# Kernel tuning notes

Hardware: AMD Instinct MI355X
Metric: run time of the kernel (lower is better)

The kernel has to match this reference:

```python
import jax, jax.numpy as jnp
import numpy as np

B, C, H, Wd = 256, 2048, 14, 14
E, A = 16, 3000  # num experts (DESC_INDEX), num answers (ANSWER_INDEX)


def setup_inputs() -> dict:
    key = jax.random.key(0)
    k1, k2, k3, k4, k5 = jax.random.split(key, 5)
    return {
        "mask": jax.random.uniform(k1, (B, 1, H, Wd), dtype=jnp.float32),
        "features": jax.random.normal(k2, (B, C, H, Wd), dtype=jnp.float32),
        "W": jax.random.normal(k3, (E, A, C), dtype=jnp.float32) * 0.02,
        "b": jax.random.normal(k4, (E, A), dtype=jnp.float32) * 0.02,
        "inst": jax.random.randint(k5, (B,), 0, E, dtype=jnp.int64),
    }


def reference(mask, features, W, b, inst):
    Bn, Cn = features.shape[0], features.shape[1]
    feat = features.reshape(Bn, Cn, -1)          # [B, C, HW]
    m = mask.reshape(Bn, 1, -1) + 1e-10          # [B, 1, HW]
    # masked weighted average pool over spatial positions
    attended = (m * feat).sum(2) / m.sum(2)      # [B, C]
    # per-sample expert Linear: compute all experts via one GEMM, then gather
    logits = jnp.einsum('bc,eac->bea', attended, W) + b[None]  # [B, E, A]
    out = jnp.take_along_axis(logits, inst[:, None, None], axis=1)[:, 0, :]  # [B, A]
    return out
```

## Files before the change

kernel.cpp:

```cpp
#include <hip/hip_runtime.h>
#include <cstdint>

#define BN   256
#define CN   2048
#define HWN  196
#define EN   16
#define AN   3000

#define TS   32
#define TA   64
#define KC   32
#define LDST 36
#define KSPLIT 4
#define KPART (CN / KSPLIT)

#define RPW  8

__global__ __launch_bounds__(256) void den_kernel(const float* __restrict__ mask,
                                                  float* __restrict__ rden) {
    int wave = blockIdx.x * 4 + (threadIdx.x >> 6);
    int lane = threadIdx.x & 63;
    float den = 0.f;
    if (lane < HWN / 4) {
        float4 m = ((const float4*)(mask + (size_t)wave * HWN))[lane];
        den = (m.x + 1e-10f) + (m.y + 1e-10f) + (m.z + 1e-10f) + (m.w + 1e-10f);
    }
    #pragma unroll
    for (int off = 32; off; off >>= 1) den += __shfl_xor(den, off, 64);
    if (lane == 0) rden[wave] = 1.0f / den;
}

__global__ __launch_bounds__(256) void pool_kernel(const float* __restrict__ mask,
                                                   const float* __restrict__ feat,
                                                   const float* __restrict__ rden,
                                                   float* __restrict__ attended) {
    int wave = blockIdx.x * 4 + (threadIdx.x >> 6);
    int lane = threadIdx.x & 63;
    int b  = wave >> 8;
    int c0 = (wave & 255) * RPW;
    bool act = lane < HWN / 4;

    float4 m = make_float4(0.f, 0.f, 0.f, 0.f);
    if (act) {
        m = ((const float4*)(mask + (size_t)b * HWN))[lane];
        m.x += 1e-10f; m.y += 1e-10f; m.z += 1e-10f; m.w += 1e-10f;
    }
    const float4* fb = (const float4*)(feat + ((size_t)b * CN + c0) * HWN);
    float4 f[RPW];
    #pragma unroll
    for (int r = 0; r < RPW; r++)
        f[r] = act ? fb[r * (HWN / 4) + lane] : make_float4(0.f, 0.f, 0.f, 0.f);
    float num[RPW];
    #pragma unroll
    for (int r = 0; r < RPW; r++)
        num[r] = m.x * f[r].x + m.y * f[r].y + m.z * f[r].z + m.w * f[r].w;
    #pragma unroll
    for (int off = 32; off; off >>= 1)
        #pragma unroll
        for (int r = 0; r < RPW; r++) num[r] += __shfl_xor(num[r], off, 64);
    if (lane == 0) {
        float rd = rden[b];
        #pragma unroll
        for (int r = 0; r < RPW; r++)
            attended[(size_t)b * CN + c0 + r] = num[r] * rd;
    }
}

__global__ void group_kernel(const int* __restrict__ inst,
                             int* __restrict__ counts,
                             int* __restrict__ lists) {
    __shared__ int cnt[EN];
    int t = threadIdx.x;
    if (t < EN) cnt[t] = 0;
    __syncthreads();
    if (t < BN) {
        int e = inst[t];
        int pos = atomicAdd(&cnt[e], 1);
        lists[e * BN + pos] = t;
    }
    __syncthreads();
    if (t < EN) counts[t] = cnt[t];
}

__global__ __launch_bounds__(256) void bias_init_kernel(const float* __restrict__ bias,
                                                        const int* __restrict__ inst,
                                                        float* __restrict__ out) {
    int b = blockIdx.x;
    int e = inst[b];
    const float4* br = (const float4*)(bias + (size_t)e * AN);
    float4* orow = (float4*)(out + (size_t)b * AN);
    for (int j = threadIdx.x; j < AN / 4; j += 256) orow[j] = br[j];
}

__global__ __launch_bounds__(128, 4) void gemm_kernel(const float* __restrict__ attended,
                                                      const float* __restrict__ W,
                                                      const int* __restrict__ counts,
                                                      const int* __restrict__ lists,
                                                      float* __restrict__ out) {
    int e  = blockIdx.y;
    int kp = blockIdx.z;
    int a0 = blockIdx.x * TA;
    int n  = counts[e];
    if (n == 0) return;
    int kbeg = kp * KPART;
    int kend = kbeg + KPART;

    __shared__ float At[TS * LDST];
    __shared__ float Wt[TA * LDST];
    __shared__ int   sid[TS];

    int t    = threadIdx.x;
    int ts   = t & 7;
    int ta   = t >> 3;
    int srow = t >> 3;
    int spos = t & 7;
    const int* lst = lists + e * BN;

    for (int s0 = 0; s0 < n; s0 += TS) {
        if (t < TS) sid[t] = (s0 + t < n) ? lst[s0 + t] : -1;

        float acc[4][4];
        #pragma unroll
        for (int i = 0; i < 4; i++)
            #pragma unroll
            for (int j = 0; j < 4; j++) acc[i][j] = 0.f;

        __syncthreads();

        float4 apre[2], wpre[4];
        #pragma unroll
        for (int r = 0; r < 2; r++) {
            int s = sid[srow + 16 * r];
            apre[r] = make_float4(0.f, 0.f, 0.f, 0.f);
            if (s >= 0)
                apre[r] = *(const float4*)(attended + (size_t)s * CN + kbeg + spos * 4);
        }
        #pragma unroll
        for (int r = 0; r < 4; r++) {
            int a = a0 + srow + 16 * r; if (a > AN - 1) a = AN - 1;
            wpre[r] = *(const float4*)(W + ((size_t)e * AN + a) * CN + kbeg + spos * 4);
        }

        for (int k0 = kbeg; k0 < kend; k0 += KC) {
            #pragma unroll
            for (int r = 0; r < 2; r++)
                *(float4*)(&At[(srow + 16 * r) * LDST + spos * 4]) = apre[r];
            #pragma unroll
            for (int r = 0; r < 4; r++)
                *(float4*)(&Wt[(srow + 16 * r) * LDST + spos * 4]) = wpre[r];
            __syncthreads();

            if (k0 + KC < kend) {
                int kn = k0 + KC;
                #pragma unroll
                for (int r = 0; r < 2; r++) {
                    int s = sid[srow + 16 * r];
                    apre[r] = make_float4(0.f, 0.f, 0.f, 0.f);
                    if (s >= 0)
                        apre[r] = *(const float4*)(attended + (size_t)s * CN + kn + spos * 4);
                }
                #pragma unroll
                for (int r = 0; r < 4; r++) {
                    int a = a0 + srow + 16 * r; if (a > AN - 1) a = AN - 1;
                    wpre[r] = *(const float4*)(W + ((size_t)e * AN + a) * CN + kn + spos * 4);
                }
            }

            #pragma unroll
            for (int kc = 0; kc < KC / 4; kc++) {
                float4 av[4], wv[4];
                #pragma unroll
                for (int i = 0; i < 4; i++)
                    av[i] = *(const float4*)(&At[(ts + 8 * i) * LDST + kc * 4]);
                #pragma unroll
                for (int j = 0; j < 4; j++)
                    wv[j] = *(const float4*)(&Wt[(ta + 16 * j) * LDST + kc * 4]);
                #pragma unroll
                for (int i = 0; i < 4; i++)
                    #pragma unroll
                    for (int j = 0; j < 4; j++) {
                        acc[i][j] += av[i].x * wv[j].x;
                        acc[i][j] += av[i].y * wv[j].y;
                        acc[i][j] += av[i].z * wv[j].z;
                        acc[i][j] += av[i].w * wv[j].w;
                    }
            }
            __syncthreads();
        }

        #pragma unroll
        for (int j = 0; j < 4; j++) {
            int a = a0 + ta + 16 * j;
            if (a < AN) {
                #pragma unroll
                for (int i = 0; i < 4; i++) {
                    int s = sid[ts + 8 * i];
                    if (s >= 0) atomicAdd(&out[(size_t)s * AN + a], acc[i][j]);
                }
            }
        }
        __syncthreads();
    }
}

extern "C" void kernel_launch(void* const* d_in, const int* in_sizes, int n_in,
                              void* d_out, int out_size, void* d_ws, size_t ws_size,
                              hipStream_t stream) {
    const float* mask = (const float*)d_in[0];
    const float* feat = (const float*)d_in[1];
    const float* W    = (const float*)d_in[2];
    const float* bias = (const float*)d_in[3];
    const int*   inst = (const int*)d_in[4];
    float* out = (float*)d_out;

    char* ws = (char*)d_ws;
    float* attended = (float*)ws;
    float* rden     = (float*)(ws + (size_t)BN * CN * sizeof(float));
    int*   counts   = (int*)(rden + BN);
    int*   lists    = counts + EN;

    den_kernel<<<BN / 4, 256, 0, stream>>>(mask, rden);
    group_kernel<<<1, 256, 0, stream>>>(inst, counts, lists);
    pool_kernel<<<BN * CN / RPW / 4, 256, 0, stream>>>(mask, feat, rden, attended);
    bias_init_kernel<<<BN, 256, 0, stream>>>(bias, inst, out);
    dim3 grid((AN + TA - 1) / TA, EN, KSPLIT);
    gemm_kernel<<<grid, 128, 0, stream>>>(attended, W, counts, lists, out);
}
```

Baseline: 868.2 us.

## Use direct global-to-LDS loads with swizzled double buffering in expert GEMM

The GEMM now uses global_load_lds builtins to move attended and W tiles straight into a double-buffered, XOR-swizzled shared-memory layout, replacing the register-staged prefetch and padded LDS. The aim is to cut register pressure and VGPR round-trips and to avoid bank conflicts. Separately, the denominator computation is folded into the pool kernel's shuffle reduction, and the grouping kernel is merged into the bias-init kernel, removing two launches. Launch bounds drop to 3 waves' worth of occupancy. Padding rows now load a real sample's data instead of zeros, but their results are still masked out at the atomic store.

```diff
diff --git a/kernel.cpp b/kernel.cpp
--- a/kernel.cpp
+++ b/kernel.cpp
@@ -10,29 +10,20 @@
 #define TS   32
 #define TA   64
 #define KC   32
-#define LDST 36
 #define KSPLIT 4
 #define KPART (CN / KSPLIT)
+#define NCHUNK (KPART / KC)
 
 #define RPW  8
 
-__global__ __launch_bounds__(256) void den_kernel(const float* __restrict__ mask,
-                                                  float* __restrict__ rden) {
-    int wave = blockIdx.x * 4 + (threadIdx.x >> 6);
-    int lane = threadIdx.x & 63;
-    float den = 0.f;
-    if (lane < HWN / 4) {
-        float4 m = ((const float4*)(mask + (size_t)wave * HWN))[lane];
-        den = (m.x + 1e-10f) + (m.y + 1e-10f) + (m.z + 1e-10f) + (m.w + 1e-10f);
-    }
-    #pragma unroll
-    for (int off = 32; off; off >>= 1) den += __shfl_xor(den, off, 64);
-    if (lane == 0) rden[wave] = 1.0f / den;
+typedef const __attribute__((address_space(1))) void gvoid_t;
+typedef __attribute__((address_space(3))) void lvoid_t;
+__device__ __forceinline__ void gll16(const float* g, float* l) {
+    __builtin_amdgcn_global_load_lds((gvoid_t*)g, (lvoid_t*)l, 16, 0, 0);
 }
 
 __global__ __launch_bounds__(256) void pool_kernel(const float* __restrict__ mask,
                                                    const float* __restrict__ feat,
-                                                   const float* __restrict__ rden,
                                                    float* __restrict__ attended) {
     int wave = blockIdx.x * 4 + (threadIdx.x >> 6);
     int lane = threadIdx.x & 63;
@@ -50,49 +41,54 @@
     #pragma unroll
     for (int r = 0; r < RPW; r++)
         f[r] = act ? fb[r * (HWN / 4) + lane] : make_float4(0.f, 0.f, 0.f, 0.f);
-    float num[RPW];
+
+    float red[RPW + 1];
     #pragma unroll
     for (int r = 0; r < RPW; r++)
-        num[r] = m.x * f[r].x + m.y * f[r].y + m.z * f[r].z + m.w * f[r].w;
+        red[r] = m.x * f[r].x + m.y * f[r].y + m.z * f[r].z + m.w * f[r].w;
+    red[RPW] = m.x + m.y + m.z + m.w;
+
     #pragma unroll
     for (int off = 32; off; off >>= 1)
         #pragma unroll
-        for (int r = 0; r < RPW; r++) num[r] += __shfl_xor(num[r], off, 64);
+        for (int r = 0; r <= RPW; r++) red[r] += __shfl_xor(red[r], off, 64);
+
     if (lane == 0) {
-        float rd = rden[b];
-        #pragma unroll
-        for (int r = 0; r < RPW; r++)
-            attended[(size_t)b * CN + c0 + r] = num[r] * rd;
-    }
-}
-
-__global__ void group_kernel(const int* __restrict__ inst,
-                             int* __restrict__ counts,
-                             int* __restrict__ lists) {
-    __shared__ int cnt[EN];
-    int t = threadIdx.x;
-    if (t < EN) cnt[t] = 0;
-    __syncthreads();
-    if (t < BN) {
-        int e = inst[t];
-        int pos = atomicAdd(&cnt[e], 1);
-        lists[e * BN + pos] = t;
-    }
-    __syncthreads();
-    if (t < EN) counts[t] = cnt[t];
-}
-
-__global__ __launch_bounds__(256) void bias_init_kernel(const float* __restrict__ bias,
-                                                        const int* __restrict__ inst,
-                                                        float* __restrict__ out) {
+        float rd = 1.0f / red[RPW];
+        float4 o0 = make_float4(red[0] * rd, red[1] * rd, red[2] * rd, red[3] * rd);
+        float4 o1 = make_float4(red[4] * rd, red[5] * rd, red[6] * rd, red[7] * rd);
+        float4* orow = (float4*)(attended + (size_t)b * CN + c0);
+        orow[0] = o0; orow[1] = o1;
+    }
+}
+
+__global__ __launch_bounds__(256) void bias_group_kernel(const float* __restrict__ bias,
+                                                         const int* __restrict__ inst,
+                                                         float* __restrict__ out,
+                                                         int* __restrict__ counts,
+                                                         int* __restrict__ lists) {
     int b = blockIdx.x;
     int e = inst[b];
     const float4* br = (const float4*)(bias + (size_t)e * AN);
     float4* orow = (float4*)(out + (size_t)b * AN);
     for (int j = threadIdx.x; j < AN / 4; j += 256) orow[j] = br[j];
-}
-
-__global__ __launch_bounds__(128, 4) void gemm_kernel(const float* __restrict__ attended,
+
+    if (blockIdx.x == 0) {
+        __shared__ int cnt[EN];
+        int t = threadIdx.x;
+        if (t < EN) cnt[t] = 0;
+        __syncthreads();
+        if (t < BN) {
+            int ee = inst[t];
+            int pos = atomicAdd(&cnt[ee], 1);
+            lists[ee * BN + pos] = t;
+        }
+        __syncthreads();
+        if (t < EN) counts[t] = cnt[t];
+    }
+}
+
+__global__ __launch_bounds__(128, 3) void gemm_kernel(const float* __restrict__ attended,
                                                       const float* __restrict__ W,
                                                       const int* __restrict__ counts,
                                                       const int* __restrict__ lists,
@@ -103,21 +99,38 @@
     int n  = counts[e];
     if (n == 0) return;
     int kbeg = kp * KPART;
-    int kend = kbeg + KPART;
-
-    __shared__ float At[TS * LDST];
-    __shared__ float Wt[TA * LDST];
-    __shared__ int   sid[TS];
+
+    __shared__ __align__(16) float tile[2][(TS + TA) * KC];
+    __shared__ int sid[TS];
 
     int t    = threadIdx.x;
     int ts   = t & 7;
     int ta   = t >> 3;
-    int srow = t >> 3;
-    int spos = t & 7;
+    int wv_  = t >> 6;
+    int lane = t & 63;
+    int r    = lane >> 3;
+    int cs   = (lane & 7) ^ r;
+
     const int* lst = lists + e * BN;
 
     for (int s0 = 0; s0 < n; s0 += TS) {
         if (t < TS) sid[t] = (s0 + t < n) ? lst[s0 + t] : -1;
+        __syncthreads();
+
+        const float* gsrc[6];
+        #pragma unroll
+        for (int q = 0; q < 6; q++) {
+            int u = wv_ * 6 + q;
+            if (u < 4) {
+                int s = sid[8 * u + r];
+                if (s < 0) s = sid[0];
+                gsrc[q] = attended + (size_t)s * CN + kbeg + cs * 4;
+            } else {
+                int a = a0 + 8 * (u - 4) + r;
+                if (a > AN - 1) a = AN - 1;
+                gsrc[q] = W + ((size_t)e * AN + a) * CN + kbeg + cs * 4;
+            }
+        }
 
         float acc[4][4];
         #pragma unroll
@@ -125,67 +138,41 @@
             #pragma unroll
             for (int j = 0; j < 4; j++) acc[i][j] = 0.f;
 
-        __syncthreads();
-
-        float4 apre[2], wpre[4];
-        #pragma unroll
-        for (int r = 0; r < 2; r++) {
-            int s = sid[srow + 16 * r];
-            apre[r] = make_float4(0.f, 0.f, 0.f, 0.f);
-            if (s >= 0)
-                apre[r] = *(const float4*)(attended + (size_t)s * CN + kbeg + spos * 4);
-        }
-        #pragma unroll
-        for (int r = 0; r < 4; r++) {
-            int a = a0 + srow + 16 * r; if (a > AN - 1) a = AN - 1;
-            wpre[r] = *(const float4*)(W + ((size_t)e * AN + a) * CN + kbeg + spos * 4);
-        }
-
-        for (int k0 = kbeg; k0 < kend; k0 += KC) {
-            #pragma unroll
-            for (int r = 0; r < 2; r++)
-                *(float4*)(&At[(srow + 16 * r) * LDST + spos * 4]) = apre[r];
-            #pragma unroll
-            for (int r = 0; r < 4; r++)
-                *(float4*)(&Wt[(srow + 16 * r) * LDST + spos * 4]) = wpre[r];
-            __syncthreads();
-
-            if (k0 + KC < kend) {
-                int kn = k0 + KC;
-                #pragma unroll
-                for (int r = 0; r < 2; r++) {
-                    int s = sid[srow + 16 * r];
-                    apre[r] = make_float4(0.f, 0.f, 0.f, 0.f);
-                    if (s >= 0)
-                        apre[r] = *(const float4*)(attended + (size_t)s * CN + kn + spos * 4);
-                }
-                #pragma unroll
-                for (int r = 0; r < 4; r++) {
-                    int a = a0 + srow + 16 * r; if (a > AN - 1) a = AN - 1;
-                    wpre[r] = *(const float4*)(W + ((size_t)e * AN + a) * CN + kn + spos * 4);
-                }
-            }
-
+        #pragma unroll
+        for (int q = 0; q < 6; q++)
+            gll16(gsrc[q], &tile[0][(wv_ * 6 + q) * 256]);
+        __syncthreads();
+
+        int cur = 0;
+        for (int ck = 0; ck < NCHUNK; ck++) {
+            if (ck + 1 < NCHUNK) {
+                #pragma unroll
+                for (int q = 0; q < 6; q++)
+                    gll16(gsrc[q] + (ck + 1) * KC, &tile[cur ^ 1][(wv_ * 6 + q) * 256]);
+            }
+
+            const float* tb = tile[cur];
             #pragma unroll
             for (int kc = 0; kc < KC / 4; kc++) {
-                float4 av[4], wv[4];
+                float4 av[4], wvv[4];
                 #pragma unroll
                 for (int i = 0; i < 4; i++)
-                    av[i] = *(const float4*)(&At[(ts + 8 * i) * LDST + kc * 4]);
+                    av[i] = *(const float4*)(tb + (ts + 8 * i) * KC + ((kc ^ ts) << 2));
                 #pragma unroll
                 for (int j = 0; j < 4; j++)
-                    wv[j] = *(const float4*)(&Wt[(ta + 16 * j) * LDST + kc * 4]);
+                    wvv[j] = *(const float4*)(tb + (TS + ta + 16 * j) * KC + ((kc ^ (ta & 7)) << 2));
                 #pragma unroll
                 for (int i = 0; i < 4; i++)
                     #pragma unroll
                     for (int j = 0; j < 4; j++) {
-                        acc[i][j] += av[i].x * wv[j].x;
-                        acc[i][j] += av[i].y * wv[j].y;
-                        acc[i][j] += av[i].z * wv[j].z;
-                        acc[i][j] += av[i].w * wv[j].w;
+                        acc[i][j] += av[i].x * wvv[j].x;
+                        acc[i][j] += av[i].y * wvv[j].y;
+                        acc[i][j] += av[i].z * wvv[j].z;
+                        acc[i][j] += av[i].w * wvv[j].w;
                     }
             }
             __syncthreads();
+            cur ^= 1;
         }
 
         #pragma unroll
@@ -215,14 +202,11 @@
 
     char* ws = (char*)d_ws;
     float* attended = (float*)ws;
-    float* rden     = (float*)(ws + (size_t)BN * CN * sizeof(float));
-    int*   counts   = (int*)(rden + BN);
+    int*   counts   = (int*)(ws + (size_t)BN * CN * sizeof(float));
     int*   lists    = counts + EN;
 
-    den_kernel<<<BN / 4, 256, 0, stream>>>(mask, rden);
-    group_kernel<<<1, 256, 0, stream>>>(inst, counts, lists);
-    pool_kernel<<<BN * CN / RPW / 4, 256, 0, stream>>>(mask, feat, rden, attended);
-    bias_init_kernel<<<BN, 256, 0, stream>>>(bias, inst, out);
+    bias_group_kernel<<<BN, 256, 0, stream>>>(bias, inst, out, counts, lists);
+    pool_kernel<<<BN * CN / RPW / 4, 256, 0, stream>>>(mask, feat, attended);
     dim3 grid((AN + TA - 1) / TA, EN, KSPLIT);
     gemm_kernel<<<grid, 128, 0, stream>>>(attended, W, counts, lists, out);
 }
```

Result: faster. 799.5 us (-7.9%).
